# Kernel optimization log

Hardware: AMD Instinct MI355X
Metric: run time of the kernel (lower is better)

## Reference

```python
import jax, jax.numpy as jnp
import numpy as np

N_NODES = 50000
N_EDGES = 800000
D_IN = 128
D_OUT = 128
NEG_SLOPE = 0.2


def setup_inputs() -> dict:
    key = jax.random.key(0)
    ks = jax.random.split(key, 6)
    stdv = 1.0 / np.sqrt(D_OUT)
    X = jax.random.normal(ks[0], (N_NODES, D_IN), dtype=jnp.float32)
    W = jax.random.uniform(ks[1], (D_IN, D_OUT), dtype=jnp.float32, minval=-stdv, maxval=stdv)
    W_r = jax.random.uniform(ks[2], (D_IN, D_OUT), dtype=jnp.float32, minval=-stdv, maxval=stdv)
    W_l = jax.random.uniform(ks[3], (D_IN, D_OUT), dtype=jnp.float32, minval=-stdv, maxval=stdv)
    src = jax.random.randint(ks[4], (N_EDGES,), 0, N_NODES, dtype=jnp.int32)
    dst = jax.random.randint(ks[5], (N_EDGES,), 0, N_NODES, dtype=jnp.int32)
    return {"X": X, "W": W, "W_r": W_r, "W_l": W_l, "src": src, "dst": dst}


def reference(X, W, W_r, W_l, src, dst):
    # Dense transforms (comb/agg feature paths)
    comb = X @ W            # [N, D_out]
    h_r = X @ W_r           # [N, D_out]
    h_l = X @ W_l           # [N, D_out]
    # SDDMM: per-edge score e_ij = dot(h_l[i], h_r[j]) at nonzeros of A
    e = jnp.sum(h_l[src] * h_r[dst], axis=-1)          # [E]
    e = jax.nn.leaky_relu(e, negative_slope=NEG_SLOPE)  # LeakyReLU(0.2) on edge values
    # SpMM aggregation: agg[i] = sum_{j in N(i)} e_ij * comb[j]
    msgs = e[:, None] * comb[dst]                       # [E, D_out]
    agg = jax.ops.segment_sum(msgs, src, num_segments=N_NODES)  # [N, D_out]
    return agg
```

## Files before the change

kernel.cpp:

```cpp
#include <hip/hip_runtime.h>
#include <hip/hip_bf16.h>

#define N_NODES 50000
#define N_EDGES 800000
#define D 128
#define NEG_SLOPE 0.2f
#define APAD 136

#define FB 196
#define BCAP 8192
#define CHUNK 2048
#define BIN_NBLK ((N_EDGES + CHUNK - 1) / CHUNK)
#define GROWS 64
#define GGRID ((N_NODES + GROWS - 1) / GROWS)
#define GEMM_LDS (D * APAD * 2 + GROWS * APAD * 2)

typedef __attribute__((ext_vector_type(8))) short bf16x8;
typedef __attribute__((ext_vector_type(4))) float f32x4;

__device__ inline unsigned short f2bf(float f) {
    union { float f; unsigned u; } v; v.f = f;
    const unsigned r = v.u + 0x7FFF + ((v.u >> 16) & 1);
    return (unsigned short)(r >> 16);
}
__device__ inline unsigned fbits(float f) { union { float f; unsigned u; } v; v.f = f; return v.u; }
__device__ inline float ffrom(unsigned u) { union { unsigned u; float f; } v; v.u = u; return v.f; }

__device__ inline void unpack8(const float4 raw, float* o) {
    const unsigned w0 = fbits(raw.x), w1 = fbits(raw.y), w2 = fbits(raw.z), w3 = fbits(raw.w);
    o[0] = ffrom(w0 << 16); o[1] = ffrom(w0 & 0xffff0000u);
    o[2] = ffrom(w1 << 16); o[3] = ffrom(w1 & 0xffff0000u);
    o[4] = ffrom(w2 << 16); o[5] = ffrom(w2 & 0xffff0000u);
    o[6] = ffrom(w3 << 16); o[7] = ffrom(w3 & 0xffff0000u);
}

__device__ __forceinline__ float rsum16(float t) {
    union { float f; int i; } u, s;
    u.f = t;
    s.i = __builtin_amdgcn_update_dpp(0, u.i, 0x128, 0xF, 0xF, true); u.f += s.f;
    s.i = __builtin_amdgcn_update_dpp(0, u.i, 0x124, 0xF, 0xF, true); u.f += s.f;
    s.i = __builtin_amdgcn_update_dpp(0, u.i, 0x4E,  0xF, 0xF, true); u.f += s.f;
    s.i = __builtin_amdgcn_update_dpp(0, u.i, 0x39,  0xF, 0xF, true); u.f += s.f;
    return u.f;
}

__device__ inline int scan256_incl(int* arr, int t, int v) {
    arr[t] = v; __syncthreads();
#pragma unroll
    for (int off = 1; off < 256; off <<= 1) {
        const int u = (t >= off) ? arr[t - off] : 0;
        __syncthreads();
        arr[t] += u;
        __syncthreads();
    }
    return arr[t];
}

__device__ __forceinline__ void stage_B_lds(unsigned short* Bs, const ushort* __restrict__ BT) {
    const int tid = threadIdx.x;
#pragma unroll
    for (int i = 0; i < 8; ++i) {
        const int idx = tid + i * 256;
        const int row = idx >> 4;
        const int c8 = (idx & 15) << 3;
        const float4 v = ((const float4*)BT)[idx];
        *(float4*)&Bs[row * APAD + c8] = v;
    }
}

template <bool OUT_F32>
__device__ __forceinline__ void mfma_from_lds(const unsigned short* Bs,
                                              const unsigned short* As,
                                              int rb, float* __restrict__ Cf,
                                              ushort* __restrict__ Cb, int nrows) {
    const int tid = threadIdx.x;
    const int w = tid >> 6, lane = tid & 63, m = lane & 15, kq = lane >> 4;
    f32x4 acc[8] = {};
    const unsigned short* Arow = &As[(w * 16 + m) * APAD + kq * 8];
#pragma unroll
    for (int kc = 0; kc < 4; ++kc) {
        const bf16x8 af = *(const bf16x8*)(Arow + kc * 32);
#pragma unroll
        for (int t2 = 0; t2 < 8; ++t2) {
            const bf16x8 bf = *(const bf16x8*)&Bs[(t2 * 16 + m) * APAD + kc * 32 + kq * 8];
            acc[t2] = __builtin_amdgcn_mfma_f32_16x16x32_bf16(af, bf, acc[t2], 0, 0, 0);
        }
    }
    const int orow0 = rb + w * 16 + kq * 4;
#pragma unroll
    for (int t2 = 0; t2 < 8; ++t2) {
#pragma unroll
        for (int r = 0; r < 4; ++r) {
            const int row = orow0 + r;
            if (row < nrows) {
                const size_t o = (size_t)row * D + t2 * 16 + m;
                if (OUT_F32) Cf[o] = acc[t2][r];
                else         Cb[o] = f2bf(acc[t2][r]);
            }
        }
    }
}

__global__ __launch_bounds__(256) void prep_kernel(const float* __restrict__ W_l,
                                                   const float* __restrict__ W_r,
                                                   const float* __restrict__ W,
                                                   ushort* __restrict__ MbT,
                                                   ushort* __restrict__ WbT,
                                                   int* __restrict__ bucket_fill) {
    if (blockIdx.x == 0) bucket_fill[threadIdx.x] = 0;
    const int a = blockIdx.x * 2 + (threadIdx.x >> 7);
    const int b2 = threadIdx.x & 127;
    float acc = 0.f;
#pragma unroll
    for (int c = 0; c < D; c += 4) {
        const float4 wl = *(const float4*)(W_l + a * D + c);
        const float4 wr = *(const float4*)(W_r + b2 * D + c);
        acc += wl.x * wr.x + wl.y * wr.y + wl.z * wr.z + wl.w * wr.w;
    }
    MbT[b2 * D + a] = f2bf(acc);
    WbT[b2 * D + a] = f2bf(W[a * D + b2]);
}

__global__ __launch_bounds__(256) void k1_kernel(const int* __restrict__ src,
                                                 const int* __restrict__ dst,
                                                 int* __restrict__ bucket_fill,
                                                 int2* __restrict__ binned,
                                                 const ushort* __restrict__ MbT,
                                                 const float4* __restrict__ Xf4,
                                                 ushort* __restrict__ Xb,
                                                 ushort* __restrict__ hMb) {
    __shared__ __align__(16) char smem[GEMM_LDS];
    const int bx = blockIdx.x;
    const int t = threadIdx.x;

    if (bx < BIN_NBLK) {
        int*  hist     = (int*)smem;
        int*  bstart   = hist + 256;
        int*  reserveS = bstart + 256;
        int*  fillL    = reserveS + 256;
        int2* pairs    = (int2*)(fillL + 256);
        int*  targ     = (int*)(pairs + CHUNK);
        const int e0 = bx * CHUNK;

        hist[t] = 0;
        __syncthreads();

        int s[8], d[8], b[8];
#pragma unroll
        for (int i = 0; i < 8; ++i) {
            const int e = e0 + i * 256 + t;
            if (e < N_EDGES) {
                s[i] = src[e]; d[i] = dst[e]; b[i] = s[i] >> 8;
                atomicAdd(&hist[b[i]], 1);
            } else b[i] = -1;
        }
        __syncthreads();
        const int hv = hist[t];
        const int incl = scan256_incl(bstart, t, hv);
        const int mystart = incl - hv;
        reserveS[t] = hv ? atomicAdd(&bucket_fill[t], hv) : 0;
        __syncthreads();
        bstart[t] = mystart;
        fillL[t] = mystart;
        __syncthreads();
#pragma unroll
        for (int i = 0; i < 8; ++i) {
            if (b[i] >= 0) {
                const int p = atomicAdd(&fillL[b[i]], 1);
                pairs[p] = make_int2(s[i], d[i]);
                const int pos = reserveS[b[i]] + (p - bstart[b[i]]);
                targ[p] = (pos < BCAP) ? (b[i] * BCAP + pos) : -1;
            }
        }
        __syncthreads();
        const int nval = min(CHUNK, N_EDGES - e0);
        for (int j = t; j < nval; j += 256)
            if (targ[j] >= 0) binned[targ[j]] = pairs[j];
    } else {
        unsigned short* Bs = (unsigned short*)smem;
        unsigned short* As = Bs + D * APAD;
        const int rb = (bx - BIN_NBLK) * GROWS;

        stage_B_lds(Bs, MbT);
#pragma unroll
        for (int i = 0; i < 4; ++i) {
            const int f2 = t + i * 256;
            const int row = f2 >> 4;
            const int c8 = (f2 & 15) << 3;
            ushort4 lo = {0, 0, 0, 0}, hi = {0, 0, 0, 0};
            if (rb + row < N_NODES) {
                const float4 a = Xf4[(size_t)(rb + row) * 32 + (c8 >> 2)];
                const float4 b = Xf4[(size_t)(rb + row) * 32 + (c8 >> 2) + 1];
                lo.x = f2bf(a.x); lo.y = f2bf(a.y); lo.z = f2bf(a.z); lo.w = f2bf(a.w);
                hi.x = f2bf(b.x); hi.y = f2bf(b.y); hi.z = f2bf(b.z); hi.w = f2bf(b.w);
                ushort* gp = Xb + (size_t)(rb + row) * D + c8;
                *(ushort4*)gp = lo;
                *(ushort4*)(gp + 4) = hi;
            }
            *(ushort4*)&As[row * APAD + c8] = lo;
            *(ushort4*)&As[row * APAD + c8 + 4] = hi;
        }
        __syncthreads();
        mfma_from_lds<false>(Bs, As, rb, nullptr, hMb, N_NODES);
    }
}

__global__ __launch_bounds__(512) void fine_kernel(const int2* __restrict__ binned,
                                                   const int* __restrict__ bucket_fill,
                                                   int* __restrict__ offsets,
                                                   int* __restrict__ sorted_dst) {
    __shared__ int cntS[256];
    __shared__ int nh[256];
    __shared__ int ex[256];
    __shared__ int fill[256];
    __shared__ int dstbuf[BCAP];
    const int b = blockIdx.x;
    const int t = threadIdx.x;

    if (t < 256) cntS[t] = (t < FB) ? bucket_fill[t] : 0;
    __syncthreads();
#pragma unroll
    for (int off = 1; off < 256; off <<= 1) {
        const int u = (t >= off && t < 256) ? cntS[t - off] : 0;
        __syncthreads();
        if (t < 256) cntS[t] += u;
        __syncthreads();
    }
    const int base = (b == 0) ? 0 : cntS[b - 1];
    int cnt = cntS[b] - base;
    if (cnt > BCAP) cnt = BCAP;

    if (t < 256) nh[t] = 0;
    __syncthreads();
    const int2* bb = binned + (size_t)b * BCAP;
    for (int e = t; e < cnt; e += 512) atomicAdd(&nh[bb[e].x & 255], 1);
    __syncthreads();
    const int v = (t < 256) ? nh[t] : 0;
    if (t < 256) ex[t] = v;
    __syncthreads();
#pragma unroll
    for (int off = 1; off < 256; off <<= 1) {
        const int u = (t >= off && t < 256) ? ex[t - off] : 0;
        __syncthreads();
        if (t < 256) ex[t] += u;
        __syncthreads();
    }
    if (t < 256) {
        const int mystart = ex[t] - v;
        const int node = b * 256 + t;
        if (node < N_NODES) offsets[node] = base + mystart;
        fill[t] = mystart;
    }
    __syncthreads();
    for (int e = t; e < cnt; e += 512) {
        const int2 sd = bb[e];
        const int p = atomicAdd(&fill[sd.x & 255], 1);
        dstbuf[p] = sd.y;
    }
    __syncthreads();
    for (int j = t; j < cnt; j += 512)
        sorted_dst[base + j] = dstbuf[j];
}

__global__ __launch_bounds__(256) void spmm_kernel(const ushort* __restrict__ hMb,
                                                   const ushort* __restrict__ Xb,
                                                   const int* __restrict__ offsets,
                                                   const int* __restrict__ sorted_dst,
                                                   ushort* __restrict__ aggXb) {
    const int wave = threadIdx.x >> 6;
    const int lane = threadIdx.x & 63;
    const int node = blockIdx.x * 4 + wave;
    const int q = lane >> 4;
    const int ql = lane & 15;

    float hm[8];
    unpack8(*(const float4*)(hMb + (size_t)node * D + ql * 8), hm);

    const int start = offsets[node];
    const int end = (node == N_NODES - 1) ? N_EDGES : offsets[node + 1];

    float acc[8] = {0.f, 0.f, 0.f, 0.f, 0.f, 0.f, 0.f, 0.f};

    int idx = start + q;
    while (idx + 12 < end) {
        const int d0 = sorted_dst[idx];
        const int d1 = sorted_dst[idx + 4];
        const int d2 = sorted_dst[idx + 8];
        const int d3 = sorted_dst[idx + 12];
        const float4 r0 = *(const float4*)(Xb + (size_t)d0 * D + ql * 8);
        const float4 r1 = *(const float4*)(Xb + (size_t)d1 * D + ql * 8);
        const float4 r2 = *(const float4*)(Xb + (size_t)d2 * D + ql * 8);
        const float4 r3 = *(const float4*)(Xb + (size_t)d3 * D + ql * 8);
        float t0 = 0.f, t1 = 0.f, t2 = 0.f, t3 = 0.f;
        {
            float x[8];
            unpack8(r0, x);
#pragma unroll
            for (int j = 0; j < 8; ++j) t0 = fmaf(hm[j], x[j], t0);
            unpack8(r1, x);
#pragma unroll
            for (int j = 0; j < 8; ++j) t1 = fmaf(hm[j], x[j], t1);
            unpack8(r2, x);
#pragma unroll
            for (int j = 0; j < 8; ++j) t2 = fmaf(hm[j], x[j], t2);
            unpack8(r3, x);
#pragma unroll
            for (int j = 0; j < 8; ++j) t3 = fmaf(hm[j], x[j], t3);
        }
        t0 = rsum16(t0);
        t1 = rsum16(t1);
        t2 = rsum16(t2);
        t3 = rsum16(t3);
        const float e0 = t0 > 0.f ? t0 : NEG_SLOPE * t0;
        const float e1 = t1 > 0.f ? t1 : NEG_SLOPE * t1;
        const float e2 = t2 > 0.f ? t2 : NEG_SLOPE * t2;
        const float e3 = t3 > 0.f ? t3 : NEG_SLOPE * t3;
        {
            float x[8];
            unpack8(r0, x);
#pragma unroll
            for (int j = 0; j < 8; ++j) acc[j] = fmaf(e0, x[j], acc[j]);
            unpack8(r1, x);
#pragma unroll
            for (int j = 0; j < 8; ++j) acc[j] = fmaf(e1, x[j], acc[j]);
            unpack8(r2, x);
#pragma unroll
            for (int j = 0; j < 8; ++j) acc[j] = fmaf(e2, x[j], acc[j]);
            unpack8(r3, x);
#pragma unroll
            for (int j = 0; j < 8; ++j) acc[j] = fmaf(e3, x[j], acc[j]);
        }
        idx += 16;
    }
    if (idx < end) {
        const int i1 = idx + 4, i2 = idx + 8;
        const bool v1 = i1 < end, v2 = i2 < end;
        const int d0 = sorted_dst[idx];
        const int d1 = sorted_dst[v1 ? i1 : idx];
        const int d2 = sorted_dst[v2 ? i2 : idx];
        const float4 r0 = *(const float4*)(Xb + (size_t)d0 * D + ql * 8);
        const float4 r1 = *(const float4*)(Xb + (size_t)d1 * D + ql * 8);
        const float4 r2 = *(const float4*)(Xb + (size_t)d2 * D + ql * 8);
        float t0 = 0.f, t1 = 0.f, t2 = 0.f;
        {
            float x[8];
            unpack8(r0, x);
#pragma unroll
            for (int j = 0; j < 8; ++j) t0 = fmaf(hm[j], x[j], t0);
            unpack8(r1, x);
#pragma unroll
            for (int j = 0; j < 8; ++j) t1 = fmaf(hm[j], x[j], t1);
            unpack8(r2, x);
#pragma unroll
            for (int j = 0; j < 8; ++j) t2 = fmaf(hm[j], x[j], t2);
        }
        t0 = rsum16(t0);
        t1 = rsum16(t1);
        t2 = rsum16(t2);
        float e0 = t0 > 0.f ? t0 : NEG_SLOPE * t0;
        float e1 = t1 > 0.f ? t1 : NEG_SLOPE * t1;
        float e2 = t2 > 0.f ? t2 : NEG_SLOPE * t2;
        e1 = v1 ? e1 : 0.f;
        e2 = v2 ? e2 : 0.f;
        {
            float x[8];
            unpack8(r0, x);
#pragma unroll
            for (int j = 0; j < 8; ++j) acc[j] = fmaf(e0, x[j], acc[j]);
            unpack8(r1, x);
#pragma unroll
            for (int j = 0; j < 8; ++j) acc[j] = fmaf(e1, x[j], acc[j]);
            unpack8(r2, x);
#pragma unroll
            for (int j = 0; j < 8; ++j) acc[j] = fmaf(e2, x[j], acc[j]);
        }
    }

#pragma unroll
    for (int j = 0; j < 8; ++j) {
        acc[j] += __shfl_xor(acc[j], 16);
        acc[j] += __shfl_xor(acc[j], 32);
    }
    if (q == 0) {
        ushort4 o0, o1;
        o0.x = f2bf(acc[0]); o0.y = f2bf(acc[1]); o0.z = f2bf(acc[2]); o0.w = f2bf(acc[3]);
        o1.x = f2bf(acc[4]); o1.y = f2bf(acc[5]); o1.z = f2bf(acc[6]); o1.w = f2bf(acc[7]);
        ushort* outp = aggXb + (size_t)node * D + ql * 8;
        *(ushort4*)outp = o0;
        *(ushort4*)(outp + 4) = o1;
    }
}

__global__ __launch_bounds__(256) void gemm2_kernel(const ushort* __restrict__ A,
                                                    const ushort* __restrict__ BT,
                                                    float* __restrict__ Cf) {
    __shared__ __align__(16) char smem[GEMM_LDS];
    unsigned short* Bs = (unsigned short*)smem;
    unsigned short* As = Bs + D * APAD;
    const int tid = threadIdx.x;
    const int rb = blockIdx.x * GROWS;

    stage_B_lds(Bs, BT);
#pragma unroll
    for (int i = 0; i < 4; ++i) {
        const int idx = tid + i * 256;
        const int row = idx >> 4;
        const int c8 = (idx & 15) << 3;
        float4 v = {0.f, 0.f, 0.f, 0.f};
        if (rb + row < N_NODES)
            v = ((const float4*)(A + (size_t)(rb + row) * D))[idx & 15];
        *(float4*)&As[row * APAD + c8] = v;
    }
    __syncthreads();
    mfma_from_lds<true>(Bs, As, rb, Cf, nullptr, N_NODES);
}

extern "C" void kernel_launch(void* const* d_in, const int* in_sizes, int n_in,
                              void* d_out, int out_size, void* d_ws, size_t ws_size,
                              hipStream_t stream) {
    const float* X   = (const float*)d_in[0];
    const float* W   = (const float*)d_in[1];
    const float* W_r = (const float*)d_in[2];
    const float* W_l = (const float*)d_in[3];
    const int* src   = (const int*)d_in[4];
    const int* dst   = (const int*)d_in[5];
    float* agg = (float*)d_out;

    ushort* Xb          = (ushort*)d_ws;
    ushort* hMb         = Xb + (size_t)N_NODES * D;
    ushort* aggXb       = hMb + (size_t)N_NODES * D;
    ushort* MbT         = aggXb + (size_t)N_NODES * D;
    ushort* WbT         = MbT + D * D;
    int*    offsets     = (int*)(WbT + D * D);
    int*    sorted_dst  = offsets + N_NODES;
    int*    bucket_fill = sorted_dst + N_EDGES;
    int2*   binned      = (int2*)(bucket_fill + 256);

    prep_kernel<<<64, 256, 0, stream>>>(W_l, W_r, W, MbT, WbT, bucket_fill);

    k1_kernel<<<BIN_NBLK + GGRID, 256, 0, stream>>>(
        src, dst, bucket_fill, binned, MbT, (const float4*)X, Xb, hMb);

    fine_kernel<<<FB, 512, 0, stream>>>(binned, bucket_fill, offsets, sorted_dst);

    spmm_kernel<<<N_NODES / 4, 256, 0, stream>>>(hMb, Xb, offsets, sorted_dst, aggXb);

    gemm2_kernel<<<GGRID, 256, 0, stream>>>(aggXb, WbT, agg);
}
```

Before: 160.7 us.

## Fuse SpMM aggregation with output GEMM via LDS-staged MFMA epilogue

Merges the SpMM kernel and the trailing GEMM into one kernel. Each 1024-thread block aggregates 16 nodes (one wave per node) into LDS as bf16, then four waves multiply that 16x128 tile by W (staged into LDS per block) with MFMA and write fp32 output. This removes the aggXb round trip through global memory and one kernel launch. In exchange every block reloads the 32KB weight into LDS, and the larger blocks with a barrier may lower occupancy.

Result: faster. 156.0 us (-2.9%).

```diff
diff --git a/kernel.cpp b/kernel.cpp
--- a/kernel.cpp
+++ b/kernel.cpp
@@ -14,6 +14,10 @@
 #define GROWS 64
 #define GGRID ((N_NODES + GROWS - 1) / GROWS)
 #define GEMM_LDS (D * APAD * 2 + GROWS * APAD * 2)
+
+#define SPMM_NODES 16
+#define SPMM_GRID (N_NODES / SPMM_NODES)
+#define SPMM_LDS ((D * APAD + SPMM_NODES * APAD) * 2)
 
 typedef __attribute__((ext_vector_type(8))) short bf16x8;
 typedef __attribute__((ext_vector_type(4))) float f32x4;
@@ -262,14 +266,29 @@
         sorted_dst[base + j] = dstbuf[j];
 }
 
-__global__ __launch_bounds__(256) void spmm_kernel(const ushort* __restrict__ hMb,
-                                                   const ushort* __restrict__ Xb,
-                                                   const int* __restrict__ offsets,
-                                                   const int* __restrict__ sorted_dst,
-                                                   ushort* __restrict__ aggXb) {
-    const int wave = threadIdx.x >> 6;
-    const int lane = threadIdx.x & 63;
-    const int node = blockIdx.x * 4 + wave;
+__global__ __launch_bounds__(1024, 8) void spmm_fused_kernel(const ushort* __restrict__ hMb,
+                                                             const ushort* __restrict__ Xb,
+                                                             const int* __restrict__ offsets,
+                                                             const int* __restrict__ sorted_dst,
+                                                             const ushort* __restrict__ WbT,
+                                                             float* __restrict__ agg) {
+    __shared__ __align__(16) char smem[SPMM_LDS];
+    unsigned short* Ws = (unsigned short*)smem;
+    unsigned short* As = Ws + D * APAD;
+    const int tid = threadIdx.x;
+
+#pragma unroll
+    for (int i = 0; i < 2; ++i) {
+        const int idx = tid + i * 1024;
+        const int row = idx >> 4;
+        const int c8 = (idx & 15) << 3;
+        const float4 v = ((const float4*)WbT)[idx];
+        *(float4*)&Ws[row * APAD + c8] = v;
+    }
+
+    const int wave = tid >> 6;
+    const int lane = tid & 63;
+    const int node = blockIdx.x * SPMM_NODES + wave;
     const int q = lane >> 4;
     const int ql = lane & 15;
 
@@ -385,34 +404,35 @@
         ushort4 o0, o1;
         o0.x = f2bf(acc[0]); o0.y = f2bf(acc[1]); o0.z = f2bf(acc[2]); o0.w = f2bf(acc[3]);
         o1.x = f2bf(acc[4]); o1.y = f2bf(acc[5]); o1.z = f2bf(acc[6]); o1.w = f2bf(acc[7]);
-        ushort* outp = aggXb + (size_t)node * D + ql * 8;
-        *(ushort4*)outp = o0;
-        *(ushort4*)(outp + 4) = o1;
-    }
-}
-
-__global__ __launch_bounds__(256) void gemm2_kernel(const ushort* __restrict__ A,
-                                                    const ushort* __restrict__ BT,
-                                                    float* __restrict__ Cf) {
-    __shared__ __align__(16) char smem[GEMM_LDS];
-    unsigned short* Bs = (unsigned short*)smem;
-    unsigned short* As = Bs + D * APAD;
-    const int tid = threadIdx.x;
-    const int rb = blockIdx.x * GROWS;
-
-    stage_B_lds(Bs, BT);
-#pragma unroll
-    for (int i = 0; i < 4; ++i) {
-        const int idx = tid + i * 256;
-        const int row = idx >> 4;
-        const int c8 = (idx & 15) << 3;
-        float4 v = {0.f, 0.f, 0.f, 0.f};
-        if (rb + row < N_NODES)
-            v = ((const float4*)(A + (size_t)(rb + row) * D))[idx & 15];
-        *(float4*)&As[row * APAD + c8] = v;
-    }
-    __syncthreads();
-    mfma_from_lds<true>(Bs, As, rb, Cf, nullptr, N_NODES);
+        *(ushort4*)&As[wave * APAD + ql * 8] = o0;
+        *(ushort4*)&As[wave * APAD + ql * 8 + 4] = o1;
+    }
+    __syncthreads();
+
+    if (wave < 4) {
+        const int m = lane & 15, kq = lane >> 4;
+        f32x4 oacc[2] = {};
+        const unsigned short* Arow = &As[m * APAD + kq * 8];
+#pragma unroll
+        for (int kc = 0; kc < 4; ++kc) {
+            const bf16x8 af = *(const bf16x8*)(Arow + kc * 32);
+#pragma unroll
+            for (int tt = 0; tt < 2; ++tt) {
+                const int t2 = wave * 2 + tt;
+                const bf16x8 bf = *(const bf16x8*)&Ws[(t2 * 16 + m) * APAD + kc * 32 + kq * 8];
+                oacc[tt] = __builtin_amdgcn_mfma_f32_16x16x32_bf16(af, bf, oacc[tt], 0, 0, 0);
+            }
+        }
+        const int rbase = blockIdx.x * SPMM_NODES + kq * 4;
+#pragma unroll
+        for (int tt = 0; tt < 2; ++tt) {
+            const int t2 = wave * 2 + tt;
+#pragma unroll
+            for (int r = 0; r < 4; ++r) {
+                agg[(size_t)(rbase + r) * D + t2 * 16 + m] = oacc[tt][r];
+            }
+        }
+    }
 }
 
 extern "C" void kernel_launch(void* const* d_in, const int* in_sizes, int n_in,
@@ -443,7 +463,6 @@
 
     fine_kernel<<<FB, 512, 0, stream>>>(binned, bucket_fill, offsets, sorted_dst);
 
-    spmm_kernel<<<N_NODES / 4, 256, 0, stream>>>(hMb, Xb, offsets, sorted_dst, aggXb);
-
-    gemm2_kernel<<<GGRID, 256, 0, stream>>>(aggXb, WbT, agg);
-}
+    spmm_fused_kernel<<<SPMM_GRID, 1024, 0, stream>>>(
+        hMb, Xb, offsets, sorted_dst, WbT, agg);
+}
```
